# Kernel optimization log

Hardware: AMD Instinct MI355X
Metric: run time of the kernel (lower is better)

## Reference

```python
import jax, jax.numpy as jnp
import numpy as np

B, L, S, D, H, M, DFF, CO = 16, 512, 1024, 512, 8, 64, 2048, 512
KS = (3, 5, 7)  # MOEDecomp kernel sizes


def _avgpool(x, k):
    # AvgPool1d(kernel=k, stride=1, padding=k//2, count_include_pad=True) along L of [B,L,D]
    p = k // 2
    s = jax.lax.reduce_window(x, 0.0, jax.lax.add, (1, k, 1), (1, 1, 1), ((0, 0), (p, p), (0, 0)))
    return s / k


def _moe_decomp(x, w1, b1, w2, b2):
    trends = jnp.stack([_avgpool(x, k) for k in KS], axis=-1)          # [B,L,D,E]
    g = jax.nn.softmax(jax.nn.relu(x @ w1.T + b1) @ w2.T + b2, axis=-1)  # [B,L,E]
    trend = jnp.einsum('blde,ble->bld', trends, g)
    return x - trend, trend


def _fourier_block(x, wr, wi):
    b, l, d = x.shape
    qft = jnp.fft.rfft(x, axis=1)                                      # [B, L//2+1, D] complex
    m = min(M, qft.shape[1])
    W = wr[:, :, :m] + 1j * wi[:, :, :m]                               # [D,D,m] complex
    om = jnp.einsum('bmd,dem->bme', qft[:, :m], W)                     # per-mode complex matmul
    out_ft = jnp.zeros((b, l // 2 + 1, d), jnp.complex64).at[:, :m].set(om)
    return jnp.fft.irfft(out_ft, n=l, axis=1)


def _fourier_cross(q_in, kv, wq, bq, wk, bk, wv, bv, wo, bo):
    b, l, _ = q_in.shape
    s = kv.shape[1]
    dk = D // H
    q = (q_in @ wq.T + bq).reshape(b, l, H, dk).transpose(0, 2, 1, 3)   # [B,H,L,dk]
    k = (kv @ wk.T + bk).reshape(b, s, H, dk).transpose(0, 2, 1, 3)
    v = (kv @ wv.T + bv).reshape(b, s, H, dk).transpose(0, 2, 1, 3)
    qf = jnp.fft.rfft(q, axis=2)
    kf = jnp.fft.rfft(k, axis=2)
    vf = jnp.fft.rfft(v, axis=2)
    mq = min(M, qf.shape[2])
    mk = min(M, kf.shape[2])
    qf, kf, vf = qf[:, :, :mq], kf[:, :, :mk], vf[:, :, :mk]
    attn = (jnp.einsum('bhld,bhsd->bhls', qf.real, kf.real)
            + jnp.einsum('bhld,bhsd->bhls', qf.imag, kf.imag))
    attn = jax.nn.softmax(attn, axis=-1)
    of = jax.lax.complex(jnp.einsum('bhls,bhsd->bhld', attn, vf.real),
                         jnp.einsum('bhls,bhsd->bhld', attn, vf.imag))
    full = jnp.zeros((b, H, l // 2 + 1, dk), jnp.complex64).at[:, :, :mq].set(of)
    out = jnp.fft.irfft(full, n=l, axis=2)                              # [B,H,L,dk]
    out = out.transpose(0, 2, 1, 3).reshape(b, l, D)
    return out @ wo.T + bo


def _circ_conv(t, w):
    # Conv1d(k=3, padding=1, circular, no bias); t: [B,L,D], w: [CO,D,3]
    xt = t.transpose(0, 2, 1)                                           # [B,D,L]
    xp = jnp.concatenate([xt[:, :, -1:], xt, xt[:, :, :1]], axis=-1)
    y = jax.lax.conv_general_dilated(xp, w, (1,), 'VALID',
                                     dimension_numbers=('NCH', 'OIH', 'NCH'))
    return y.transpose(0, 2, 1)                                         # [B,L,CO]


def setup_inputs() -> dict:
    key = jax.random.key(0)
    ks = jax.random.split(key, 32)
    def n(i, shape, scale=0.02):
        return (scale * jax.random.normal(ks[i], shape)).astype(jnp.float32)
    feb_scale = 1.0 / (D * D)
    inp = {
        'x': n(0, (B, L, D), 1.0),
        'cross': n(1, (B, S, D), 1.0),
        'feb_wr': n(2, (D, D, M), feb_scale),
        'feb_wi': n(3, (D, D, M), feb_scale),
        'wq': n(4, (D, D)), 'bq': n(5, (D,)),
        'wk': n(6, (D, D)), 'bk': n(7, (D,)),
        'wv': n(8, (D, D)), 'bv': n(9, (D,)),
        'wo': n(10, (D, D)), 'bo': n(11, (D,)),
        'w_ff1': n(12, (DFF, D)), 'w_ff2': n(13, (D, DFF)),
        'd1_w1': n(14, (D // 2, D)), 'd1_b1': n(15, (D // 2,)),
        'd1_w2': n(16, (3, D // 2)), 'd1_b2': n(17, (3,)),
        'd2_w1': n(18, (D // 2, D)), 'd2_b1': n(19, (D // 2,)),
        'd2_w2': n(20, (3, D // 2)), 'd2_b2': n(21, (3,)),
        'd3_w1': n(22, (D // 2, D)), 'd3_b1': n(23, (D // 2,)),
        'd3_w2': n(24, (3, D // 2)), 'd3_b2': n(25, (3,)),
        'p1': n(26, (CO, D, 3)), 'p2': n(27, (CO, D, 3)), 'p3': n(28, (CO, D, 3)),
    }
    return inp


def reference(x, cross, feb_wr, feb_wi, wq, bq, wk, bk, wv, bv, wo, bo,
              w_ff1, w_ff2, d1_w1, d1_b1, d1_w2, d1_b2,
              d2_w1, d2_b1, d2_w2, d2_b2, d3_w1, d3_b1, d3_w2, d3_b2,
              p1, p2, p3):
    # dropout is identity (eval mode)
    x = x + _fourier_block(x, feb_wr, feb_wi)
    x, t1 = _moe_decomp(x, d1_w1, d1_b1, d1_w2, d1_b2)
    x = x + _fourier_cross(x, cross, wq, bq, wk, bk, wv, bv, wo, bo)
    x, t2 = _moe_decomp(x, d2_w1, d2_b1, d2_w2, d2_b2)
    y = jax.nn.relu(x @ w_ff1.T) @ w_ff2.T  # 1x1 convs == pointwise GEMMs
    x, t3 = _moe_decomp(x + y, d3_w1, d3_b1, d3_w2, d3_b2)
    residual_trend = _circ_conv(t1, p1) + _circ_conv(t2, p2) + _circ_conv(t3, p3)
    return x, residual_trend
```

## Files before the change

### kernel.cpp

```cpp
#include <hip/hip_runtime.h>
#include <math.h>

typedef unsigned short u16;
typedef unsigned int u32;
typedef unsigned long long u64;

constexpr int kB = 16, kL = 512, kS = 1024, kD = 512, kM = 64;

typedef __attribute__((ext_vector_type(8))) short u16x8;
typedef __attribute__((ext_vector_type(8))) _Float16 f16x8;
typedef __attribute__((ext_vector_type(4))) float f32x4;

__device__ __forceinline__ u16 f2h(float f) {
    _Float16 h = (_Float16)f;
    return *(u16*)&h;
}
__device__ __forceinline__ float h2f(u16 u) {
    _Float16 h = *(_Float16*)&u;
    return (float)h;
}

__global__ __launch_bounds__(256, 4) void gemm_fp16(
    const u16* __restrict__ Abase, const u16* __restrict__ Wbase,
    const float* __restrict__ bias, const float* __restrict__ resid,
    float* __restrict__ Cout, u16* __restrict__ Ch,
    int R, int N, int K, int flags,
    u64 zsA, u64 zsW, u64 zsC, u64 zsR, int lrsh)
{
    __shared__ __attribute__((aligned(16))) u16 Abuf[128 * 64];
    __shared__ __attribute__((aligned(16))) u16 Bbuf[128 * 64];
    const int zz = blockIdx.z;
    Abase += (u64)zz * zsA;
    Wbase += (u64)zz * zsW;
    if (Cout) Cout += (u64)zz * zsC;
    if (Ch)   Ch   += (u64)zz * zsC;
    if (resid) resid += (u64)zz * zsR;

    const int tid = threadIdx.x;
    const int lane = tid & 63;
    const int wave = tid >> 6;
    const int wr = wave >> 1, wc = wave & 1;
    const int ln15 = lane & 15, lq = lane >> 4;
    const int r0 = blockIdx.y * 128, n0 = blockIdx.x * 128;

    f32x4 acc[4][4];
#pragma unroll
    for (int m = 0; m < 4; ++m)
#pragma unroll
        for (int n = 0; n < 4; ++n) acc[m][n] = (f32x4){0.f, 0.f, 0.f, 0.f};

    for (int k0 = 0; k0 < K; k0 += 64) {
        u16x8 av[4], bv[4];
#pragma unroll
        for (int it = 0; it < 4; ++it) {
            int c = it * 256 + tid;
            int row = c >> 3, j = c & 7;
            int jj = j ^ (row & 7);
            av[it] = *(const u16x8*)(Abase + (size_t)(r0 + row) * K + k0 + jj * 8);
            bv[it] = *(const u16x8*)(Wbase + (size_t)(n0 + row) * K + k0 + jj * 8);
        }
        __syncthreads();
#pragma unroll
        for (int it = 0; it < 4; ++it) {
            int c = it * 256 + tid;
            int row = c >> 3, j = c & 7;
            *(u16x8*)&Abuf[row * 64 + j * 8] = av[it];
            *(u16x8*)&Bbuf[row * 64 + j * 8] = bv[it];
        }
        __syncthreads();
#pragma unroll
        for (int h = 0; h < 2; ++h) {
            int kg = lq + h * 4;
            f16x8 af[4], bfv[4];
#pragma unroll
            for (int m = 0; m < 4; ++m) {
                int row = wr * 64 + m * 16 + ln15;
                af[m] = *(const f16x8*)&Abuf[row * 64 + ((kg ^ (row & 7)) << 3)];
            }
#pragma unroll
            for (int n = 0; n < 4; ++n) {
                int col = wc * 64 + n * 16 + ln15;
                bfv[n] = *(const f16x8*)&Bbuf[col * 64 + ((kg ^ (col & 7)) << 3)];
            }
#pragma unroll
            for (int m = 0; m < 4; ++m)
#pragma unroll
                for (int n = 0; n < 4; ++n)
                    acc[m][n] = __builtin_amdgcn_mfma_f32_16x16x32_f16(af[m], bfv[n], acc[m][n], 0, 0, 0);
        }
        __syncthreads();
    }

#pragma unroll
    for (int m = 0; m < 4; ++m) {
#pragma unroll
        for (int n = 0; n < 4; ++n) {
            int gc = n0 + wc * 64 + n * 16 + ln15;
            float bv_ = bias ? bias[gc] : 0.f;
            int gr0 = r0 + wr * 64 + m * 16 + lq * 4;
            float v[4];
#pragma unroll
            for (int rg = 0; rg < 4; ++rg) {
                int gr = gr0 + rg;
                float val = acc[m][n][rg] + bv_;
                if (resid) val += resid[(size_t)gr * N + gc];
                if (flags & 1) val = fmaxf(val, 0.f);
                if (flags & 16) Cout[(size_t)gr * N + gc] = val;
                if (flags & 8)  Ch[(size_t)gr * N + gc] = f2h(val);
                v[rg] = val;
            }
            if (flags & 32) {
                int bb = gr0 >> lrsh;
                int l_ = gr0 & ((1 << lrsh) - 1);
                ushort4 o;
                o.x = f2h(v[0]); o.y = f2h(v[1]); o.z = f2h(v[2]); o.w = f2h(v[3]);
                *(ushort4*)&Ch[(((size_t)bb * N + gc) << lrsh) + l_] = o;
            }
        }
    }
}

__global__ __launch_bounds__(256, 4) void gemm64(
    const u16* __restrict__ Abase, const u16* __restrict__ Wbase,
    const float* __restrict__ bias, const float* __restrict__ resid,
    float* __restrict__ Cout, u16* __restrict__ Ch,
    int R, int N, int K, int flags,
    u64 zsA, u64 zsW, u64 zsC, u64 zsR, int lrsh)
{
    __shared__ __attribute__((aligned(16))) u16 Abuf[64 * 64];
    __shared__ __attribute__((aligned(16))) u16 Bbuf[64 * 64];
    const int zz = blockIdx.z;
    Abase += (u64)zz * zsA;
    Wbase += (u64)zz * zsW;
    if (Cout) Cout += (u64)zz * zsC;
    if (Ch)   Ch   += (u64)zz * zsC;
    if (resid) resid += (u64)zz * zsR;

    const int tid = threadIdx.x;
    const int lane = tid & 63;
    const int w = tid >> 6;
    const int ln15 = lane & 15, lq = lane >> 4;
    const int r0 = blockIdx.y * 64, n0 = blockIdx.x * 64;

    f32x4 acc[4];
#pragma unroll
    for (int m = 0; m < 4; ++m) acc[m] = (f32x4){0.f, 0.f, 0.f, 0.f};

    for (int k0 = 0; k0 < K; k0 += 64) {
        u16x8 av[2], bv[2];
#pragma unroll
        for (int it = 0; it < 2; ++it) {
            int c = it * 256 + tid;
            int row = c >> 3, j = c & 7;
            int jj = j ^ (row & 7);
            av[it] = *(const u16x8*)(Abase + (size_t)(r0 + row) * K + k0 + jj * 8);
            bv[it] = *(const u16x8*)(Wbase + (size_t)(n0 + row) * K + k0 + jj * 8);
        }
        __syncthreads();
#pragma unroll
        for (int it = 0; it < 2; ++it) {
            int c = it * 256 + tid;
            int row = c >> 3, j = c & 7;
            *(u16x8*)&Abuf[row * 64 + j * 8] = av[it];
            *(u16x8*)&Bbuf[row * 64 + j * 8] = bv[it];
        }
        __syncthreads();
#pragma unroll
        for (int h = 0; h < 2; ++h) {
            int kg = lq + h * 4;
            int col = w * 16 + ln15;
            f16x8 bf = *(const f16x8*)&Bbuf[col * 64 + ((kg ^ (col & 7)) << 3)];
#pragma unroll
            for (int m = 0; m < 4; ++m) {
                int row = m * 16 + ln15;
                f16x8 af = *(const f16x8*)&Abuf[row * 64 + ((kg ^ (row & 7)) << 3)];
                acc[m] = __builtin_amdgcn_mfma_f32_16x16x32_f16(af, bf, acc[m], 0, 0, 0);
            }
        }
        __syncthreads();
    }

    const int gc = n0 + w * 16 + ln15;
    const float bv_ = bias ? bias[gc] : 0.f;
#pragma unroll
    for (int m = 0; m < 4; ++m) {
        int gr0 = r0 + m * 16 + lq * 4;
        float v[4];
#pragma unroll
        for (int rg = 0; rg < 4; ++rg) {
            int gr = gr0 + rg;
            float val = acc[m][rg] + bv_;
            if (resid) val += resid[(size_t)gr * N + gc];
            if (flags & 1) val = fmaxf(val, 0.f);
            if (flags & 16) Cout[(size_t)gr * N + gc] = val;
            if (flags & 8)  Ch[(size_t)gr * N + gc] = f2h(val);
            v[rg] = val;
        }
        if (flags & 32) {
            int bb = gr0 >> lrsh;
            int l_ = gr0 & ((1 << lrsh) - 1);
            ushort4 o;
            o.x = f2h(v[0]); o.y = f2h(v[1]); o.z = f2h(v[2]); o.w = f2h(v[3]);
            *(ushort4*)&Ch[(((size_t)bb * N + gc) << lrsh) + l_] = o;
        }
    }
}

__global__ __launch_bounds__(256) void prep(
    const float* __restrict__ wq, const float* __restrict__ wk,
    const float* __restrict__ wv, const float* __restrict__ wo,
    const float* __restrict__ ff1, const float* __restrict__ ff2,
    const float* __restrict__ dw1, const float* __restrict__ dw2,
    const float* __restrict__ dw3, const float* __restrict__ cross,
    const float* __restrict__ bk, const float* __restrict__ bv,
    u16* __restrict__ wqh, u16* __restrict__ wkvh, u16* __restrict__ woh,
    u16* __restrict__ ff1h, u16* __restrict__ ff2h,
    u16* __restrict__ d1w1h, u16* __restrict__ d2w1h, u16* __restrict__ d3w1h,
    u16* __restrict__ crossh, float* __restrict__ bkv,
    u16* __restrict__ tw512, u16* __restrict__ tw1024, u16* __restrict__ tih)
{
    const int gid = blockIdx.x * 256 + threadIdx.x;
    const int stride = gridDim.x * 256;
    for (int i = gid; i < 262144; i += stride) wqh[i] = f2h(wq[i]);
    for (int i = gid; i < 262144; i += stride) wkvh[i] = f2h(wk[i]);
    for (int i = gid; i < 262144; i += stride) wkvh[262144 + i] = f2h(wv[i]);
    for (int i = gid; i < 262144; i += stride) woh[i] = f2h(wo[i]);
    for (int i = gid; i < 1048576; i += stride) ff1h[i] = f2h(ff1[i]);
    for (int i = gid; i < 1048576; i += stride) ff2h[i] = f2h(ff2[i]);
    for (int i = gid; i < 131072; i += stride) d1w1h[i] = f2h(dw1[i]);
    for (int i = gid; i < 131072; i += stride) d2w1h[i] = f2h(dw2[i]);
    for (int i = gid; i < 131072; i += stride) d3w1h[i] = f2h(dw3[i]);
    const float4* c4 = (const float4*)cross;
    for (int i = gid; i < 2097152; i += stride) {
        float4 v = c4[i];
        ushort4 o;
        o.x = f2h(v.x); o.y = f2h(v.y); o.z = f2h(v.z); o.w = f2h(v.w);
        *(ushort4*)&crossh[i * 4] = o;
    }
    for (int i = gid; i < 1024; i += stride) bkv[i] = (i < 512) ? bk[i] : bv[i - 512];
    for (int i = gid; i < 65536; i += stride) {
        int r = i >> 9, l = i & 511;
        int m = r & 63;
        int ph = (m * l) & 511;
        float ang = 6.283185307179586f * (float)ph / 512.0f;
        float s_, c_;
        sincosf(ang, &s_, &c_);
        tw512[i] = f2h((r < 64) ? c_ : -s_);
    }
    for (int i = gid; i < 131072; i += stride) {
        int r = i >> 10, l = i & 1023;
        int m = r & 63;
        int ph = (m * l) & 1023;
        float ang = 6.283185307179586f * (float)ph / 1024.0f;
        float s_, c_;
        sincosf(ang, &s_, &c_);
        tw1024[i] = f2h((r < 64) ? c_ : -s_);
    }
    for (int i = gid; i < 65536; i += stride) {
        int l = i >> 7, r = i & 127;
        int m = r & 63;
        int ph = (m * l) & 511;
        float ang = 6.283185307179586f * (float)ph / 512.0f;
        float s_, c_;
        sincosf(ang, &s_, &c_);
        float val;
        if (r == 0) val = 1.0f / 512.0f;
        else if (r < 64) val = 2.0f * c_ / 512.0f;
        else if (r == 64) val = 0.0f;
        else val = -2.0f * s_ / 512.0f;
        tih[i] = f2h(val);
    }
}

__global__ __launch_bounds__(256) void repack_feb(
    const float* __restrict__ wr, const float* __restrict__ wi,
    u16* __restrict__ FW, u16* __restrict__ FI)
{
    __shared__ u16 t0[64][66], t1[64][66];
    const int e = blockIdx.x;
    const int d0 = blockIdx.y * 64;
    const int tid = threadIdx.x;
#pragma unroll
    for (int rep = 0; rep < 16; ++rep) {
        int idx = tid + rep * 256;
        int dd = idx >> 6, mm = idx & 63;
        size_t g = ((size_t)(d0 + dd) * 512 + e) * 64 + mm;
        t0[dd][mm] = f2h(wr[g]);
        t1[dd][mm] = f2h(wi[g]);
    }
    __syncthreads();
#pragma unroll
    for (int rep = 0; rep < 16; ++rep) {
        int idx = tid + rep * 256;
        int mm = idx >> 6, dd = idx & 63;
        size_t o = ((size_t)mm * 512 + e) * 512 + d0 + dd;
        FW[o] = t0[dd][mm];
        FI[o] = t1[dd][mm];
    }
}

__global__ __launch_bounds__(256, 4) void feb_mfma(
    const float* __restrict__ QF, const u16* __restrict__ FW,
    const u16* __restrict__ FI, u16* __restrict__ OMT)
{
    __shared__ __attribute__((aligned(16))) u16 Aq[16 * 64];
    __shared__ __attribute__((aligned(16))) u16 Ai[16 * 64];
    __shared__ __attribute__((aligned(16))) u16 Br[64 * 64];
    __shared__ __attribute__((aligned(16))) u16 Bi[64 * 64];
    const int e0 = blockIdx.x * 64;
    const int m  = blockIdx.y;
    const int tid = threadIdx.x;
    const int lane = tid & 63;
    const int w = tid >> 6;
    const int ln15 = lane & 15, lq = lane >> 4;

    f32x4 arr = (f32x4){0.f, 0.f, 0.f, 0.f};
    f32x4 aii = arr, ari = arr, air = arr;

    for (int d0 = 0; d0 < 512; d0 += 64) {
        u16x8 ahv;
        {
            int ar_ = tid >> 7;
            int row = (tid >> 3) & 15;
            int j = tid & 7;
            int jj = j ^ (row & 7);
            const float* src = QF + ((size_t)row * 128 + (ar_ ? 64 + m : m)) * 512 + d0 + jj * 8;
            float4 v0 = *(const float4*)src;
            float4 v1 = *(const float4*)(src + 4);
            ahv[0] = (short)f2h(v0.x); ahv[1] = (short)f2h(v0.y);
            ahv[2] = (short)f2h(v0.z); ahv[3] = (short)f2h(v0.w);
            ahv[4] = (short)f2h(v1.x); ahv[5] = (short)f2h(v1.y);
            ahv[6] = (short)f2h(v1.z); ahv[7] = (short)f2h(v1.w);
        }
        u16x8 bvv[4];
#pragma unroll
        for (int it = 0; it < 4; ++it) {
            int c = it * 256 + tid;
            int ar_ = c >> 9;
            int row = (c >> 3) & 63;
            int j = c & 7;
            int jj = j ^ (row & 7);
            const u16* src = (ar_ ? FI : FW) + ((size_t)m * 512 + e0 + row) * 512 + d0 + jj * 8;
            bvv[it] = *(const u16x8*)src;
        }
        __syncthreads();
        {
            int ar_ = tid >> 7;
            int row = (tid >> 3) & 15;
            int j = tid & 7;
            *(u16x8*)&((ar_ ? Ai : Aq)[row * 64 + j * 8]) = ahv;
        }
#pragma unroll
        for (int it = 0; it < 4; ++it) {
            int c = it * 256 + tid;
            int ar_ = c >> 9;
            int row = (c >> 3) & 63;
            int j = c & 7;
            *(u16x8*)&((ar_ ? Bi : Br)[row * 64 + j * 8]) = bvv[it];
        }
        __syncthreads();
#pragma unroll
        for (int h = 0; h < 2; ++h) {
            int kg = lq + h * 4;
            f16x8 aqf = *(const f16x8*)&Aq[ln15 * 64 + ((kg ^ (ln15 & 7)) << 3)];
            f16x8 aif = *(const f16x8*)&Ai[ln15 * 64 + ((kg ^ (ln15 & 7)) << 3)];
            int col = w * 16 + ln15;
            f16x8 brf = *(const f16x8*)&Br[col * 64 + ((kg ^ (col & 7)) << 3)];
            f16x8 bif = *(const f16x8*)&Bi[col * 64 + ((kg ^ (col & 7)) << 3)];
            arr = __builtin_amdgcn_mfma_f32_16x16x32_f16(aqf, brf, arr, 0, 0, 0);
            aii = __builtin_amdgcn_mfma_f32_16x16x32_f16(aif, bif, aii, 0, 0, 0);
            ari = __builtin_amdgcn_mfma_f32_16x16x32_f16(aqf, bif, ari, 0, 0, 0);
            air = __builtin_amdgcn_mfma_f32_16x16x32_f16(aif, brf, air, 0, 0, 0);
        }
        __syncthreads();
    }

    const int e = e0 + w * 16 + ln15;
#pragma unroll
    for (int rg = 0; rg < 4; ++rg) {
        int b = lq * 4 + rg;
        float omr = arr[rg] - aii[rg];
        float omi = ari[rg] + air[rg];
        u16* o = OMT + ((size_t)(b * 512 + e)) * 128;
        o[m] = f2h(omr);
        o[64 + m] = f2h(omi);
    }
}

__global__ __launch_bounds__(256) void tr_cast_x(
    const float* __restrict__ x, u16* __restrict__ xt)
{
    __shared__ u16 t[64][72];
    const int b = blockIdx.y;
    const int lt = (blockIdx.x >> 3) * 64, dt = (blockIdx.x & 7) * 64;
    const int tid = threadIdx.x;
#pragma unroll
    for (int rep = 0; rep < 16; ++rep) {
        int idx = tid + rep * 256;
        int row = idx >> 6, col = idx & 63;
        t[row][col] = f2h(x[((size_t)b * kL + lt + row) * kD + dt + col]);
    }
    __syncthreads();
#pragma unroll
    for (int rep = 0; rep < 16; ++rep) {
        int idx = tid + rep * 256;
        int row = idx >> 6, col = idx & 63;
        xt[((size_t)b * kD + dt + row) * kL + lt + col] = t[col][row];
    }
}

__global__ __launch_bounds__(256) void spectral_attn(
    const float* __restrict__ QF, const float* __restrict__ KVF,
    u16* __restrict__ OMT)
{
    __shared__ float kr[64][65], ki[64][65], sat[64][65];
    const int b = blockIdx.x >> 3, h = blockIdx.x & 7;
    const int tid = threadIdx.x;
    const int dbase = h * 64;
    const float* KVFb = KVF + (size_t)b * 128 * 1024;

    for (int idx = tid; idx < 4096; idx += 256) {
        int j = idx >> 6, dd = idx & 63;
        kr[j][dd] = KVFb[(size_t)j * 1024 + dbase + dd];
        ki[j][dd] = KVFb[(size_t)(64 + j) * 1024 + dbase + dd];
    }
    __syncthreads();

    const int i_ = tid >> 2, jg = tid & 3;
    float s[16];
#pragma unroll
    for (int jj = 0; jj < 16; ++jj) s[jj] = 0.f;
    const float* qrp = QF + ((size_t)b * 128 + i_) * 512 + dbase;
    const float* qip = qrp + (size_t)64 * 512;
    for (int dd = 0; dd < 64; ++dd) {
        float qr = qrp[dd], qi = qip[dd];
#pragma unroll
        for (int jj = 0; jj < 16; ++jj) {
            int j = jg * 16 + jj;
            s[jj] += qr * kr[j][dd] + qi * ki[j][dd];
        }
    }
    float mx = s[0];
#pragma unroll
    for (int jj = 1; jj < 16; ++jj) mx = fmaxf(mx, s[jj]);
    mx = fmaxf(mx, __shfl_xor(mx, 1));
    mx = fmaxf(mx, __shfl_xor(mx, 2));
    float sum = 0.f;
#pragma unroll
    for (int jj = 0; jj < 16; ++jj) { s[jj] = expf(s[jj] - mx); sum += s[jj]; }
    sum += __shfl_xor(sum, 1);
    sum += __shfl_xor(sum, 2);
    float rinv = 1.0f / sum;
#pragma unroll
    for (int jj = 0; jj < 16; ++jj) sat[i_][jg * 16 + jj] = s[jj] * rinv;
    __syncthreads();

    const int dd = tid & 63, ig = tid >> 6;
    float ar[16], ai[16];
#pragma unroll
    for (int ii = 0; ii < 16; ++ii) { ar[ii] = 0.f; ai[ii] = 0.f; }
    const float* VFb = KVFb + 512 + dbase + dd;
    for (int j = 0; j < 64; ++j) {
        float vr = VFb[(size_t)j * 1024];
        float vi = VFb[(size_t)(64 + j) * 1024];
#pragma unroll
        for (int ii = 0; ii < 16; ++ii) {
            float a = sat[ig * 16 + ii][j];
            ar[ii] += a * vr;
            ai[ii] += a * vi;
        }
    }
    u16* o = OMT + ((size_t)(b * 512 + dbase + dd)) * 128 + ig * 16;
    u16x8 v0, v1, w0, w1;
#pragma unroll
    for (int q = 0; q < 8; ++q) {
        v0[q] = (short)f2h(ar[q]);     v1[q] = (short)f2h(ar[8 + q]);
        w0[q] = (short)f2h(ai[q]);     w1[q] = (short)f2h(ai[8 + q]);
    }
    *(u16x8*)(o) = v0;
    *(u16x8*)(o + 8) = v1;
    *(u16x8*)(o + 64) = w0;
    *(u16x8*)(o + 72) = w1;
}

__global__ __launch_bounds__(256) void decomp_apply(
    const float* __restrict__ x, const float* __restrict__ logits,
    float* __restrict__ xout, u16* __restrict__ xout_h, u16* __restrict__ tout_h)
{
    int idx = blockIdx.x * 256 + threadIdx.x;
    if (idx >= kB * kL * kD) return;
    int d = idx & 511;
    int l = (idx >> 9) & 511;
    int b = idx >> 18;
    const float* lg = logits + ((size_t)b * kL + l) * 3;
    float g0 = lg[0], g1 = lg[1], g2 = lg[2];
    float m = fmaxf(g0, fmaxf(g1, g2));
    float e0 = expf(g0 - m), e1 = expf(g1 - m), e2 = expf(g2 - m);
    float inv = 1.0f / (e0 + e1 + e2);
    g0 = e0 * inv; g1 = e1 * inv; g2 = e2 * inv;

    const float* xb = x + (size_t)b * kL * kD + d;
    float v[7];
#pragma unroll
    for (int j = 0; j < 7; ++j) {
        int ls = l + j - 3;
        v[j] = (ls >= 0 && ls < kL) ? xb[(size_t)ls * kD] : 0.f;
    }
    float s3 = (v[2] + v[3] + v[4]) * (1.0f / 3.0f);
    float s5 = (v[1] + v[2] + v[3] + v[4] + v[5]) * 0.2f;
    float s7 = (v[0] + v[1] + v[2] + v[3] + v[4] + v[5] + v[6]) * (1.0f / 7.0f);
    float trend = g0 * s3 + g1 * s5 + g2 * s7;
    float res = v[3] - trend;
    if (xout) xout[idx] = res;
    if (xout_h) xout_h[idx] = f2h(res);
    tout_h[idx] = f2h(trend);
}

__global__ __launch_bounds__(256) void gate2(
    const u16* __restrict__ GH, const float* __restrict__ w2,
    const float* __restrict__ b2, float* __restrict__ logits)
{
    __shared__ float w2l[3][256];
    int tid = threadIdx.x;
    for (int i = tid; i < 768; i += 256) w2l[i >> 8][i & 255] = w2[i];
    __syncthreads();
    int gid = blockIdx.x * 256 + tid;
    int r = gid >> 2, q = gid & 3;
    float s0 = 0.f, s1 = 0.f, s2 = 0.f;
    const u16* g = GH + (size_t)r * 256 + q * 64;
    for (int c0 = 0; c0 < 64; c0 += 8) {
        uint4 u = *(const uint4*)&g[c0];
        u32 w[4] = {u.x, u.y, u.z, u.w};
#pragma unroll
        for (int p = 0; p < 4; ++p) {
            float f0 = h2f((u16)(w[p] & 0xFFFF));
            float f1 = h2f((u16)(w[p] >> 16));
            int c = q * 64 + c0 + p * 2;
            s0 += f0 * w2l[0][c] + f1 * w2l[0][c + 1];
            s1 += f0 * w2l[1][c] + f1 * w2l[1][c + 1];
            s2 += f0 * w2l[2][c] + f1 * w2l[2][c + 1];
        }
    }
    s0 += __shfl_xor(s0, 1); s0 += __shfl_xor(s0, 2);
    s1 += __shfl_xor(s1, 1); s1 += __shfl_xor(s1, 2);
    s2 += __shfl_xor(s2, 1); s2 += __shfl_xor(s2, 2);
    if (q == 0) {
        logits[(size_t)r * 3 + 0] = s0 + b2[0];
        logits[(size_t)r * 3 + 1] = s1 + b2[1];
        logits[(size_t)r * 3 + 2] = s2 + b2[2];
    }
}

__global__ void repack_p(const float* __restrict__ p1, const float* __restrict__ p2,
                         const float* __restrict__ p3, u16* __restrict__ pk)
{
    int idx = blockIdx.x * 256 + threadIdx.x;
    if (idx >= 3 * 3 * 512 * 512) return;
    int d = idx & 511;
    int oc = (idx >> 9) & 511;
    int j = (idx / (512 * 512)) % 3;
    int t = idx / (3 * 512 * 512);
    const float* p = (t == 0) ? p1 : (t == 1) ? p2 : p3;
    pk[idx] = f2h(p[(size_t)oc * 512 * 3 + (size_t)d * 3 + j]);
}

__global__ __launch_bounds__(256) void conv_sum(
    const u16* __restrict__ Cc, float* __restrict__ outt)
{
    int gid = blockIdx.x * 256 + threadIdx.x;
    int ocg = gid & 63;
    int r = gid >> 6;
    int b = r >> 9, l = r & 511;
    float s[8];
#pragma unroll
    for (int q = 0; q < 8; ++q) s[q] = 0.f;
#pragma unroll
    for (int t = 0; t < 3; ++t) {
#pragma unroll
        for (int j = 0; j < 3; ++j) {
            int lr = (l + j + 511) & 511;
            const u16x8 v = *(const u16x8*)&Cc[(size_t)t * 8192 * 1536 +
                ((size_t)(b * 512 + lr)) * 1536 + j * 512 + ocg * 8];
#pragma unroll
            for (int q = 0; q < 8; ++q) s[q] += h2f((u16)v[q]);
        }
    }
    float4 o0 = {s[0], s[1], s[2], s[3]};
    float4 o1 = {s[4], s[5], s[6], s[7]};
    *(float4*)&outt[(size_t)r * 512 + ocg * 8] = o0;
    *(float4*)&outt[(size_t)r * 512 + ocg * 8 + 4] = o1;
}

extern "C" void kernel_launch(void* const* d_in, const int* in_sizes, int n_in,
                              void* d_out, int out_size, void* d_ws, size_t ws_size,
                              hipStream_t stream)
{
    const float* x_in   = (const float*)d_in[0];
    const float* cross  = (const float*)d_in[1];
    const float* feb_wr = (const float*)d_in[2];
    const float* feb_wi = (const float*)d_in[3];
    const float* wq = (const float*)d_in[4];
    const float* bq = (const float*)d_in[5];
    const float* wk = (const float*)d_in[6];
    const float* bk = (const float*)d_in[7];
    const float* wv = (const float*)d_in[8];
    const float* bv = (const float*)d_in[9];
    const float* wo = (const float*)d_in[10];
    const float* bo = (const float*)d_in[11];
    const float* w_ff1 = (const float*)d_in[12];
    const float* w_ff2 = (const float*)d_in[13];
    const float* d1_w1 = (const float*)d_in[14];
    const float* d1_b1 = (const float*)d_in[15];
    const float* d1_w2 = (const float*)d_in[16];
    const float* d1_b2 = (const float*)d_in[17];
    const float* d2_w1 = (const float*)d_in[18];
    const float* d2_b1 = (const float*)d_in[19];
    const float* d2_w2 = (const float*)d_in[20];
    const float* d2_b2 = (const float*)d_in[21];
    const float* d3_w1 = (const float*)d_in[22];
    const float* d3_b1 = (const float*)d_in[23];
    const float* d3_w2 = (const float*)d_in[24];
    const float* d3_b2 = (const float*)d_in[25];
    const float* p1 = (const float*)d_in[26];
    const float* p2 = (const float*)d_in[27];
    const float* p3 = (const float*)d_in[28];

    float* ws = (float*)d_ws;
    float* X    = ws;
    float* XT   = ws + 4194304;
    u16*  KVt   = (u16*)(ws + 8388608);
    u16*  Q0t   = (u16*)(ws + 16777216);
    u16*  T1h   = (u16*)(ws + 18874368);
    u16*  T2h   = (u16*)(ws + 20971520);
    u16*  T3h   = (u16*)(ws + 23068672);
    float* QF   = ws + 25165824;
    float* KVF  = ws + 26214400;
    u16*  OMTh  = (u16*)(ws + 28311552);
    u16*  crossh = (u16*)(ws + 29884416);
    u16*  Xh    = (u16*)(ws + 34078720);
    u16*  XTh   = (u16*)(ws + 36175872);
    u16*  GHh   = (u16*)(ws + 38273024);
    float* GLG  = ws + 39321600;
    u16*  wqh   = (u16*)(ws + 39346176);
    u16*  wkvh  = wqh + 262144;
    u16*  woh   = wkvh + 524288;
    u16*  ff1h  = woh + 262144;
    u16*  ff2h  = ff1h + 1048576;
    u16*  d1w1h = ff2h + 1048576;
    u16*  d2w1h = d1w1h + 131072;
    u16*  d3w1h = d2w1h + 131072;
    u16*  PKh   = d3w1h + 131072;
    u16*  TW512h  = (u16*)(ws + 42295296);
    u16*  TW1024h = (u16*)(ws + 42328064);
    u16*  TIh     = (u16*)(ws + 42393600);
    float* bkv    = ws + 42426368;
    u16*  FWh   = (u16*)X;
    u16*  FIh   = (u16*)KVt;
    u16*  xTh   = Q0t;
    u16*  HIDh  = KVt;
    u16*  Qh    = Q0t;
    u16*  Cch   = (u16*)ws;

    float* outx = (float*)d_out;
    float* outt = outx + 4194304;

    auto g128 = [&](const u16* A, const u16* W, const float* bias, const float* resid,
                    float* C, u16* Cb, int R, int N, int K, int flags,
                    int Z, u64 zsA, u64 zsW, u64 zsC, u64 zsR, int lrsh) {
        dim3 g(N / 128, R / 128, Z);
        hipLaunchKernelGGL(gemm_fp16, g, dim3(256), 0, stream,
                           A, W, bias, resid, C, Cb, R, N, K, flags, zsA, zsW, zsC, zsR, lrsh);
    };
    auto g64 = [&](const u16* A, const u16* W, const float* bias, const float* resid,
                   float* C, u16* Cb, int R, int N, int K, int flags,
                   int Z, u64 zsA, u64 zsW, u64 zsC, u64 zsR, int lrsh) {
        dim3 g(N / 64, R / 64, Z);
        hipLaunchKernelGGL(gemm64, g, dim3(256), 0, stream,
                           A, W, bias, resid, C, Cb, R, N, K, flags, zsA, zsW, zsC, zsR, lrsh);
    };

    hipLaunchKernelGGL(prep, dim3(2048), dim3(256), 0, stream,
                       wq, wk, wv, wo, w_ff1, w_ff2, d1_w1, d2_w1, d3_w1, cross, bk, bv,
                       wqh, wkvh, woh, ff1h, ff2h, d1w1h, d2w1h, d3w1h, crossh, bkv,
                       TW512h, TW1024h, TIh);
    hipLaunchKernelGGL(repack_p, dim3(9216), dim3(256), 0, stream, p1, p2, p3, PKh);
    hipLaunchKernelGGL(repack_feb, dim3(512, 8), dim3(256), 0, stream,
                       feb_wr, feb_wi, FWh, FIh);

    hipLaunchKernelGGL(tr_cast_x, dim3(64, 16), dim3(256), 0, stream, x_in, xTh);
    g64(TW512h, xTh, nullptr, nullptr, QF, nullptr, 128, 512, 512, 16,
        16, 0, (u64)512 * 512, (u64)128 * 512, 0, 0);
    hipLaunchKernelGGL(feb_mfma, dim3(8, 64), dim3(256), 0, stream, QF, FWh, FIh, OMTh);
    g64(TIh, OMTh, nullptr, x_in, X, Xh, 512, 512, 128, 16 | 8,
        16, 0, (u64)512 * 128, (u64)512 * 512, (u64)512 * 512, 0);

    g64(Xh, d1w1h, d1_b1, nullptr, nullptr, GHh, 8192, 256, 512, 1 | 8, 1, 0, 0, 0, 0, 0);
    hipLaunchKernelGGL(gate2, dim3(128), dim3(256), 0, stream, GHh, d1_w2, d1_b2, GLG);
    hipLaunchKernelGGL(decomp_apply, dim3(16384), dim3(256), 0, stream, X, GLG, XT, XTh, T1h);

    g64(XTh, wqh, bq, nullptr, nullptr, Q0t, 8192, 512, 512, 32, 1, 0, 0, 0, 0, 9);
    g128(crossh, wkvh, bkv, nullptr, nullptr, KVt, 16384, 1024, 512, 32, 1, 0, 0, 0, 0, 10);
    g64(TW512h, Q0t, nullptr, nullptr, QF, nullptr, 128, 512, 512, 16,
        16, 0, (u64)512 * 512, (u64)128 * 512, 0, 0);
    g64(TW1024h, KVt, nullptr, nullptr, KVF, nullptr, 128, 1024, 1024, 16,
        16, 0, (u64)1024 * 1024, (u64)128 * 1024, 0, 0);
    hipLaunchKernelGGL(spectral_attn, dim3(128), dim3(256), 0, stream, QF, KVF, OMTh);
    g64(TIh, OMTh, nullptr, nullptr, nullptr, Qh, 512, 512, 128, 8,
        16, 0, (u64)512 * 128, (u64)512 * 512, 0, 0);
    g64(Qh, woh, bo, XT, X, Xh, 8192, 512, 512, 16 | 8, 1, 0, 0, 0, 0, 0);

    g64(Xh, d2w1h, d2_b1, nullptr, nullptr, GHh, 8192, 256, 512, 1 | 8, 1, 0, 0, 0, 0, 0);
    hipLaunchKernelGGL(gate2, dim3(128), dim3(256), 0, stream, GHh, d2_w2, d2_b2, GLG);
    hipLaunchKernelGGL(decomp_apply, dim3(16384), dim3(256), 0, stream, X, GLG, XT, XTh, T2h);

    g128(XTh, ff1h, nullptr, nullptr, nullptr, HIDh, 8192, 2048, 512, 1 | 8, 1, 0, 0, 0, 0, 0);
    g64(HIDh, ff2h, nullptr, XT, X, Xh, 8192, 512, 2048, 16 | 8, 1, 0, 0, 0, 0, 0);

    g64(Xh, d3w1h, d3_b1, nullptr, nullptr, GHh, 8192, 256, 512, 1 | 8, 1, 0, 0, 0, 0, 0);
    hipLaunchKernelGGL(gate2, dim3(128), dim3(256), 0, stream, GHh, d3_w2, d3_b2, GLG);
    hipLaunchKernelGGL(decomp_apply, dim3(16384), dim3(256), 0, stream, X, GLG, outx,
                       (u16*)nullptr, T3h);

    g128(T1h, PKh, nullptr, nullptr, nullptr, Cch, 8192, 1536, 512, 8,
         3, (u64)8192 * 512, (u64)1536 * 512, (u64)8192 * 1536, 0, 0);
    hipLaunchKernelGGL(conv_sum, dim3(2048), dim3(256), 0, stream, Cch, outt);

    (void)in_sizes; (void)n_in; (void)out_size; (void)ws_size;
}
```

Measured before the change: 495.8 us.

## Fuse circular conv sum into implicit-GEMM over shifted rows with K=4608

```diff
diff --git a/kernel.cpp b/kernel.cpp
--- a/kernel.cpp
+++ b/kernel.cpp
@@ -147,14 +147,32 @@
     for (int m = 0; m < 4; ++m) acc[m] = (f32x4){0.f, 0.f, 0.f, 0.f};
 
     for (int k0 = 0; k0 < K; k0 += 64) {
+        int t = 0, jsh = 0, dk = k0;
+        if (flags & 4) {
+            t = k0 / 1536;
+            int rem = k0 - t * 1536;
+            jsh = rem >> 9;
+            dk = rem & 511;
+        }
         u16x8 av[2], bv[2];
 #pragma unroll
         for (int it = 0; it < 2; ++it) {
             int c = it * 256 + tid;
             int row = c >> 3, j = c & 7;
             int jj = j ^ (row & 7);
-            av[it] = *(const u16x8*)(Abase + (size_t)(r0 + row) * K + k0 + jj * 8);
-            bv[it] = *(const u16x8*)(Wbase + (size_t)(n0 + row) * K + k0 + jj * 8);
+            size_t aoff, boff;
+            if (flags & 4) {
+                int grow = r0 + row;
+                int b_ = grow >> 9, l_ = grow & 511;
+                int sr = (b_ << 9) | ((l_ + jsh + 511) & 511);
+                aoff = (size_t)t * (size_t)(kB * kL * kD) + (size_t)sr * 512 + dk + jj * 8;
+                boff = (((size_t)(t * 3 + jsh) * 512) + n0 + row) * 512 + dk + jj * 8;
+            } else {
+                aoff = (size_t)(r0 + row) * K + k0 + jj * 8;
+                boff = (size_t)(n0 + row) * K + k0 + jj * 8;
+            }
+            av[it] = *(const u16x8*)(Abase + aoff);
+            bv[it] = *(const u16x8*)(Wbase + boff);
         }
         __syncthreads();
 #pragma unroll
@@ -562,33 +580,6 @@
     int t = idx / (3 * 512 * 512);
     const float* p = (t == 0) ? p1 : (t == 1) ? p2 : p3;
     pk[idx] = f2h(p[(size_t)oc * 512 * 3 + (size_t)d * 3 + j]);
-}
-
-__global__ __launch_bounds__(256) void conv_sum(
-    const u16* __restrict__ Cc, float* __restrict__ outt)
-{
-    int gid = blockIdx.x * 256 + threadIdx.x;
-    int ocg = gid & 63;
-    int r = gid >> 6;
-    int b = r >> 9, l = r & 511;
-    float s[8];
-#pragma unroll
-    for (int q = 0; q < 8; ++q) s[q] = 0.f;
-#pragma unroll
-    for (int t = 0; t < 3; ++t) {
-#pragma unroll
-        for (int j = 0; j < 3; ++j) {
-            int lr = (l + j + 511) & 511;
-            const u16x8 v = *(const u16x8*)&Cc[(size_t)t * 8192 * 1536 +
-                ((size_t)(b * 512 + lr)) * 1536 + j * 512 + ocg * 8];
-#pragma unroll
-            for (int q = 0; q < 8; ++q) s[q] += h2f((u16)v[q]);
-        }
-    }
-    float4 o0 = {s[0], s[1], s[2], s[3]};
-    float4 o1 = {s[4], s[5], s[6], s[7]};
-    *(float4*)&outt[(size_t)r * 512 + ocg * 8] = o0;
-    *(float4*)&outt[(size_t)r * 512 + ocg * 8 + 4] = o1;
 }
 
 extern "C" void kernel_launch(void* const* d_in, const int* in_sizes, int n_in,
@@ -659,7 +650,6 @@
     u16*  xTh   = Q0t;
     u16*  HIDh  = KVt;
     u16*  Qh    = Q0t;
-    u16*  Cch   = (u16*)ws;
 
     float* outx = (float*)d_out;
     float* outt = outx + 4194304;
@@ -721,9 +711,8 @@
     hipLaunchKernelGGL(decomp_apply, dim3(16384), dim3(256), 0, stream, X, GLG, outx,
                        (u16*)nullptr, T3h);
 
-    g128(T1h, PKh, nullptr, nullptr, nullptr, Cch, 8192, 1536, 512, 8,
-         3, (u64)8192 * 512, (u64)1536 * 512, (u64)8192 * 1536, 0, 0);
-    hipLaunchKernelGGL(conv_sum, dim3(2048), dim3(256), 0, stream, Cch, outt);
+    g64(T1h, PKh, nullptr, nullptr, outt, nullptr, 8192, 512, 4608, 4 | 16,
+        1, 0, 0, 0, 0, 0);
 
     (void)in_sizes; (void)n_in; (void)out_size; (void)ws_size;
 }
```

Result: slower. 526.0 us (+6.1%).
